# Performance work log

Hardware: AMD Instinct MI355X
Metric: run time of the kernel (lower is better)

Reference implementation:

```python
import jax, jax.numpy as jnp
import numpy as np

B, D, H, L, A, NH = 32768, 512, 512, 64, 4, 4
HD = L // NH  # head dim
TEMPS = jnp.array([1.5, 0.5, 1.0, 0.8], dtype=jnp.float32)  # explorer/exploiter/validator/integrator


def setup_inputs() -> dict:
    key = jax.random.key(0)
    ks = jax.random.split(key, 32)
    s = 0.05
    n = lambda k, shp: jax.random.normal(k, shp, dtype=jnp.float32) * s
    return {
        'x': jax.random.normal(ks[0], (B, D), dtype=jnp.float32),
        'eps': jax.random.normal(ks[1], (B, A, L), dtype=jnp.float32),
        'W1': n(ks[2], (H, D)), 'b1': n(ks[3], (H,)),
        'W2': n(ks[4], (H, H)), 'b2': n(ks[5], (H,)),
        'muW': n(ks[6], (A, L, H)), 'mub': n(ks[7], (A, L)),
        'lvW': n(ks[8], (A, L, H)), 'lvb': n(ks[9], (A, L)),
        'Wqkv': n(ks[10], (3 * L, L)), 'bqkv': n(ks[11], (3 * L,)),
        'Wo': n(ks[12], (L, L)), 'bo': n(ks[13], (L,)),
        'Wc': n(ks[14], (L, A * L)), 'bc': n(ks[15], (L,)),
        'Wd1': n(ks[16], (H, L)), 'bd1': n(ks[17], (H,)),
        'Wd2': n(ks[18], (H, H)), 'bd2': n(ks[19], (H,)),
        'Wd3': n(ks[20], (D, H)), 'bd3': n(ks[21], (D,)),
    }


def reference(x, eps, W1, b1, W2, b2, muW, mub, lvW, lvb,
              Wqkv, bqkv, Wo, bo, Wc, bc, Wd1, bd1, Wd2, bd2, Wd3, bd3):
    b = x.shape[0]
    # shared encoder backbone: Linear-ReLU-Linear-ReLU
    h = jax.nn.relu(x @ W1.T + b1)
    h = jax.nn.relu(h @ W2.T + b2)
    # per-agent heads, batched over agent axis a
    mus = jnp.einsum('bh,alh->bal', h, muW) + mub                      # (B,A,L)
    logvars = jnp.einsum('bh,alh->bal', h, lvW) + lvb + jnp.log(TEMPS)[:, None]
    std = jnp.exp(0.5 * logvars)
    z = mus + eps * std * TEMPS[:, None]                               # (B,A,L)
    # multihead self-attention across the A agents (seq_len = A)
    qkv = z @ Wqkv.T + bqkv                                            # (B,A,3L)
    q, k, v = jnp.split(qkv, 3, axis=-1)
    q = q.reshape(b, A, NH, HD)
    k = k.reshape(b, A, NH, HD)
    v = v.reshape(b, A, NH, HD)
    scores = jnp.einsum('bqnh,bknh->bnqk', q, k) / jnp.sqrt(jnp.float32(HD))
    attn = jax.nn.softmax(scores, axis=-1)
    ctx = jnp.einsum('bnqk,bknh->bqnh', attn, v).reshape(b, A, L)
    z_att = ctx @ Wo.T + bo                                            # (B,A,L)
    # consensus over flattened agent latents
    z_consensus = z_att.reshape(b, A * L) @ Wc.T + bc                  # (B,L)

    def decode(zz):
        d = jax.nn.relu(zz @ Wd1.T + bd1)
        d = jax.nn.relu(d @ Wd2.T + bd2)
        return d @ Wd3.T + bd3

    x_recon = decode(z_consensus)                                      # (B,D)
    agent_recons = decode(z)                                           # (B,A,D)
    # stack consensus recon with per-agent recons: (B, A+1, D)
    return jnp.concatenate([x_recon[:, None, :], agent_recons], axis=1)
```

## Files before the change

### kernel.cpp

```cpp
#include <hip/hip_runtime.h>

typedef __bf16 bf16_t;
typedef __bf16 bf16x8 __attribute__((ext_vector_type(8)));
typedef __bf16 bf16x4 __attribute__((ext_vector_type(4)));
typedef float  f32x4  __attribute__((ext_vector_type(4)));

#define MFMA16(a,b,c) __builtin_amdgcn_mfma_f32_16x16x32_bf16((a),(b),(c),0,0,0)
#define GLOBAL_AS __attribute__((address_space(1)))
#define LDS_AS    __attribute__((address_space(3)))

__device__ __forceinline__ bf16x8 lds_read8(const bf16_t* base, int row, int k, int rowB) {
    int byte = row * rowB + (k << 1);
    byte ^= ((row & 7) << 4);
    return *(const bf16x8*)((const char*)base + byte);
}
__device__ __forceinline__ void lds_write8B(bf16_t* base, int row, int col, int rowB, bf16x4 v) {
    int byte = row * rowB + (col << 1);
    byte ^= ((row & 7) << 4);
    *(bf16x4*)((char*)base + byte) = v;
}
__device__ __forceinline__ bf16x4 lds_read8B(const bf16_t* base, int row, int col, int rowB) {
    int byte = row * rowB + (col << 1);
    byte ^= ((row & 7) << 4);
    return *(const bf16x4*)((const char*)base + byte);
}
__device__ __forceinline__ void lds_write1(bf16_t* base, int row, int col, int rowB, float v) {
    int byte = row * rowB + (col << 1);
    byte ^= ((row & 7) << 4);
    *(bf16_t*)((char*)base + byte) = (bf16_t)v;
}
__device__ __forceinline__ void lds_write16B(bf16_t* base, int row, int colbyte, int rowB, bf16x8 v) {
    int byte = row * rowB + colbyte;
    byte ^= ((row & 7) << 4);
    *(bf16x8*)((char*)base + byte) = v;
}
__device__ __forceinline__ bf16x8 lds_read16B(const bf16_t* base, int row, int colbyte, int rowB) {
    int byte = row * rowB + colbyte;
    byte ^= ((row & 7) << 4);
    return *(const bf16x8*)((const char*)base + byte);
}

__device__ __forceinline__ void gload_lds16(const void* g, void* l) {
    __builtin_amdgcn_global_load_lds((const GLOBAL_AS void*)g, (LDS_AS void*)l, 16, 0, 0);
}
__device__ __forceinline__ void stageW(const bf16_t* __restrict__ Wt, int tile,
                                       char* wbuf, int bufIdx, int wave, int lane) {
    const char* s = (const char*)Wt + (size_t)tile * 32768 + wave * 4096 + lane * 16;
    char* d = wbuf + bufIdx * 32768 + wave * 4096;
#pragma unroll
    for (int c = 0; c < 4; ++c)
        gload_lds16(s + c * 1024, d + c * 1024);
}

template<int NS, bool CONT, int TB>
__device__ __forceinline__ void layer_gl(f32x4 (&acc)[4][4],
    const bf16_t* act, char* wbuf,
    const bf16_t* __restrict__ Wt, const bf16_t* __restrict__ Wn,
    int wave, int lane, int n0, int l15, int lhi)
{
#pragma unroll
    for (int s = 0; s < NS; ++s) {
        if (s == NS - 1 && !CONT) {
            asm volatile("s_waitcnt vmcnt(0)" ::: "memory");
        } else {
            asm volatile("s_waitcnt vmcnt(4)" ::: "memory");
        }
        __builtin_amdgcn_s_barrier();
        if (s + 2 < NS)  stageW(Wt, s + 2,      wbuf, (TB + s + 2) % 3, wave, lane);
        else if (CONT)   stageW(Wn, s + 2 - NS, wbuf, (TB + s + 2) % 3, wave, lane);
        const char* bb = wbuf + ((TB + s) % 3) * 32768 + lhi * 8192;
        bf16x8 a[4], b[4];
#pragma unroll
        for (int cf = 0; cf < 4; ++cf)
            b[cf] = *(const bf16x8*)(bb + (n0 + cf * 16 + l15) * 16);
#pragma unroll
        for (int rf = 0; rf < 4; ++rf)
            a[rf] = lds_read8(act, rf * 16 + l15, s * 32 + lhi * 8, 1024);
#pragma unroll
        for (int rf = 0; rf < 4; ++rf)
#pragma unroll
            for (int cf = 0; cf < 4; ++cf)
                acc[rf][cf] = MFMA16(b[cf], a[rf], acc[rf][cf]);
    }
}

__device__ __forceinline__ void zero4(f32x4 (&acc)[4][4]) {
#pragma unroll
    for (int rf = 0; rf < 4; ++rf)
#pragma unroll
        for (int cf = 0; cf < 4; ++cf)
            acc[rf][cf] = f32x4{0.f, 0.f, 0.f, 0.f};
}

template<bool RELU>
__device__ __forceinline__ void epi_lds(const f32x4 (&acc)[4][4], const float* __restrict__ bias,
    bf16_t* dst, int rowB, int n0, int l15, int lhi)
{
#pragma unroll
    for (int cf = 0; cf < 4; ++cf) {
        const int c0 = n0 + cf * 16 + lhi * 4;
        float4 b4 = *(const float4*)(bias + c0);
#pragma unroll
        for (int rf = 0; rf < 4; ++rf) {
            float v0 = acc[rf][cf][0] + b4.x;
            float v1 = acc[rf][cf][1] + b4.y;
            float v2 = acc[rf][cf][2] + b4.z;
            float v3 = acc[rf][cf][3] + b4.w;
            if (RELU) {
                v0 = fmaxf(v0, 0.f); v1 = fmaxf(v1, 0.f);
                v2 = fmaxf(v2, 0.f); v3 = fmaxf(v3, 0.f);
            }
            bf16x4 p = { (bf16_t)v0, (bf16_t)v1, (bf16_t)v2, (bf16_t)v3 };
            lds_write8B(dst, rf * 16 + l15, c0, rowB, p);
        }
    }
}

__device__ __forceinline__ void epi_global(const f32x4 (&acc)[4][4], const float* __restrict__ bias,
    float* __restrict__ out, long row0, int n0, int l15, int lhi)
{
#pragma unroll
    for (int cf = 0; cf < 4; ++cf) {
        const int c0 = n0 + cf * 16 + lhi * 4;
        float4 b4 = *(const float4*)(bias + c0);
#pragma unroll
        for (int rf = 0; rf < 4; ++rf) {
            float4 o = { acc[rf][cf][0] + b4.x, acc[rf][cf][1] + b4.y,
                         acc[rf][cf][2] + b4.z, acc[rf][cf][3] + b4.w };
            *(float4*)(out + (row0 + rf * 16 + l15) * 512 + c0) = o;
        }
    }
}

__device__ __forceinline__ void decode_tile(int m, int& n, int& k) {
    int s = m >> 14, r = m & 16383;
    int kg = r >> 12, q = r & 4095;
    n = q >> 3;
    k = (s << 5) + (kg << 3) + (q & 7);
}
__global__ __launch_bounds__(256) void cast_kernel(
    const float* __restrict__ W1, const float* __restrict__ W2,
    const float* __restrict__ muW, const float* __restrict__ lvW,
    const float* __restrict__ Wqkv, const float* __restrict__ Wo,
    const float* __restrict__ Wc, const float* __restrict__ Wd1,
    const float* __restrict__ Wd2, const float* __restrict__ Wd3,
    bf16_t* __restrict__ dst)
{
    int i = blockIdx.x * 256 + threadIdx.x;
    float val;
    int n, k;
    if (i < 262144) {
        decode_tile(i, n, k);                     val = W1[n * 512 + k];
    } else if (i < 524288) {
        decode_tile(i - 262144, n, k);            val = W2[n * 512 + k];
    } else if (i < 786432) {
        decode_tile(i - 524288, n, k);
        val = (n < 256) ? muW[n * 512 + k] : lvW[(n - 256) * 512 + k];
    } else if (i < 798720) { val = Wqkv[i - 786432]; }
    else if (i < 802816)   { val = Wo[i - 798720]; }
    else if (i < 819200)   { val = Wc[i - 802816]; }
    else if (i < 851968) {
        decode_tile(i - 819200, n, k);            val = Wd1[n * 64 + k];
    } else if (i < 1114112) {
        decode_tile(i - 851968, n, k);            val = Wd2[n * 512 + k];
    } else {
        decode_tile(i - 1114112, n, k);           val = Wd3[n * 512 + k];
    }
    dst[i] = (bf16_t)val;
}

__global__ __launch_bounds__(512, 2) void enc_kernel(
    const float* __restrict__ x, const float* __restrict__ eps,
    const bf16_t* __restrict__ W1t, const float* __restrict__ b1,
    const bf16_t* __restrict__ W2t, const float* __restrict__ b2,
    const bf16_t* __restrict__ Ht,  const float* __restrict__ mub,
    const float* __restrict__ lvb,  bf16_t* __restrict__ zout)
{
    __shared__ bf16_t act[64 * 512];
    __shared__ alignas(16) char wbuf[3 * 32768];
    const int t = threadIdx.x;
    const int wave = t >> 6, lane = t & 63, l15 = lane & 15, lhi = lane >> 4;
    const int n0 = wave * 64;
    const size_t r0 = (size_t)blockIdx.x * 64;

    stageW(W1t, 0, wbuf, 0, wave, lane);
    stageW(W1t, 1, wbuf, 1, wave, lane);

    for (int it = 0; it < 16; ++it) {
        int flat = it * 512 + t;
        int row = flat >> 7, c4 = flat & 127;
        float4 v = ((const float4*)(x + (r0 + row) * 512))[c4];
        bf16x4 h = { (bf16_t)v.x, (bf16_t)v.y, (bf16_t)v.z, (bf16_t)v.w };
        int byte = (row << 10) + (c4 << 3);
        byte ^= ((row & 7) << 4);
        *(bf16x4*)((char*)act + byte) = h;
    }
    asm volatile("s_waitcnt lgkmcnt(0)" ::: "memory");

    f32x4 acc[4][4];
    zero4(acc);
    layer_gl<16, true, 0>(acc, act, wbuf, W1t, W2t, wave, lane, n0, l15, lhi);
    __builtin_amdgcn_s_barrier();
    epi_lds<true>(acc, b1, act, 1024, n0, l15, lhi);
    asm volatile("s_waitcnt lgkmcnt(0)" ::: "memory");
    __builtin_amdgcn_s_barrier();

    zero4(acc);
    layer_gl<16, true, 1>(acc, act, wbuf, W2t, Ht, wave, lane, n0, l15, lhi);
    __builtin_amdgcn_s_barrier();
    epi_lds<true>(acc, b2, act, 1024, n0, l15, lhi);
    asm volatile("s_waitcnt lgkmcnt(0)" ::: "memory");
    __builtin_amdgcn_s_barrier();

    zero4(acc);
    layer_gl<16, false, 2>(acc, act, wbuf, Ht, (const bf16_t*)nullptr, wave, lane, n0, l15, lhi);
    __builtin_amdgcn_s_barrier();
    epi_lds<false>(acc, (n0 < 256) ? mub : (lvb - 256), act, 1024, n0, l15, lhi);
    asm volatile("s_waitcnt lgkmcnt(0)" ::: "memory");
    __builtin_amdgcn_s_barrier();

    const int cc = (t & 63) * 4;
    const int ag = cc >> 6;
    const float tp = (ag == 0) ? 1.8371173070873836f
                   : (ag == 1) ? 0.35355339059327373f
                   : (ag == 2) ? 1.0f
                               : 0.7155417527999327f;
    const int rb = t >> 6;
    for (int it = 0; it < 8; ++it) {
        int row = it * 8 + rb;
        bf16x4 mu4 = lds_read8B(act, row, cc, 1024);
        bf16x4 lv4 = lds_read8B(act, row, cc + 256, 1024);
        float4 ep4 = *(const float4*)(eps + (r0 + row) * 256 + cc);
        bf16x4 zo;
        zo[0] = (bf16_t)fmaf(ep4.x * tp, expf(0.5f * (float)lv4[0]), (float)mu4[0]);
        zo[1] = (bf16_t)fmaf(ep4.y * tp, expf(0.5f * (float)lv4[1]), (float)mu4[1]);
        zo[2] = (bf16_t)fmaf(ep4.z * tp, expf(0.5f * (float)lv4[2]), (float)mu4[2]);
        zo[3] = (bf16_t)fmaf(ep4.w * tp, expf(0.5f * (float)lv4[3]), (float)mu4[3]);
        *(bf16x4*)(zout + (r0 + row) * 256 + cc) = zo;
    }
}

__global__ __launch_bounds__(512) void attn_kernel(
    const bf16_t* __restrict__ z,
    const bf16_t* __restrict__ Wqkvb, const float* __restrict__ bqkv,
    const bf16_t* __restrict__ Wob,   const float* __restrict__ bo,
    const bf16_t* __restrict__ Wcb,   const float* __restrict__ bc,
    bf16_t* __restrict__ zcb)
{
    __shared__ bf16_t zt[256 * 64];
    __shared__ bf16_t qt[256 * 192];
    const int t = threadIdx.x;
    const size_t s0 = (size_t)blockIdx.x * 64;

    for (int it = 0; it < 4; ++it) {
        int ch = it * 512 + t;
        int r = ch >> 3, cc = ch & 7;
        bf16x8 v = *(const bf16x8*)(z + s0 * 256 + r * 64 + cc * 8);
        lds_write16B(zt, r, cc * 16, 128, v);
    }
    __syncthreads();
    const int wave = t >> 6, lane = t & 63, l15 = lane & 15, lhi = lane >> 4;
    const int rbase = wave * 32;

    for (int cc = 0; cc < 4; ++cc) {
        f32x4 acc[2][3] = {};
#pragma unroll
        for (int ks = 0; ks < 2; ++ks) {
            int k = ks * 32 + lhi * 8;
            bf16x8 a0 = lds_read8(zt, rbase + l15, k, 128);
            bf16x8 a1 = lds_read8(zt, rbase + 16 + l15, k, 128);
#pragma unroll
            for (int cf = 0; cf < 3; ++cf) {
                bf16x8 b = *(const bf16x8*)(Wqkvb + (cc * 48 + cf * 16 + l15) * 64 + k);
                acc[0][cf] = MFMA16(a0, b, acc[0][cf]);
                acc[1][cf] = MFMA16(a1, b, acc[1][cf]);
            }
        }
#pragma unroll
        for (int cf = 0; cf < 3; ++cf) {
            int col = cc * 48 + cf * 16 + l15;
            float bs = bqkv[col];
#pragma unroll
            for (int rf = 0; rf < 2; ++rf)
#pragma unroll
                for (int r = 0; r < 4; ++r)
                    lds_write1(qt, rbase + rf * 16 + lhi * 4 + r, col, 384, acc[rf][cf][r] + bs);
        }
    }
    __syncthreads();

    if (t < 256) {
        const int sl = t >> 2, head = t & 3;
        bf16x8 qv[4][2], kv[4][2], vv[4][2];
#pragma unroll
        for (int a2 = 0; a2 < 4; ++a2) {
            int r = sl * 4 + a2;
#pragma unroll
            for (int i = 0; i < 2; ++i) {
                qv[a2][i] = lds_read16B(qt, r, head * 32 + 16 * i, 384);
                kv[a2][i] = lds_read16B(qt, r, 128 + head * 32 + 16 * i, 384);
                vv[a2][i] = lds_read16B(qt, r, 256 + head * 32 + 16 * i, 384);
            }
        }
        float sc[4][4];
#pragma unroll
        for (int qa = 0; qa < 4; ++qa)
#pragma unroll
            for (int ka = 0; ka < 4; ++ka) {
                float s = 0.f;
#pragma unroll
                for (int i = 0; i < 2; ++i)
#pragma unroll
                    for (int j = 0; j < 8; ++j)
                        s += (float)qv[qa][i][j] * (float)kv[ka][i][j];
                sc[qa][ka] = s * 0.25f;
            }
#pragma unroll
        for (int qa = 0; qa < 4; ++qa) {
            float m = fmaxf(fmaxf(sc[qa][0], sc[qa][1]), fmaxf(sc[qa][2], sc[qa][3]));
            float e[4], sum = 0.f;
#pragma unroll
            for (int ka = 0; ka < 4; ++ka) { e[ka] = expf(sc[qa][ka] - m); sum += e[ka]; }
            float inv = 1.f / sum;
#pragma unroll
            for (int i = 0; i < 2; ++i) {
                bf16x8 cv;
#pragma unroll
                for (int j = 0; j < 8; ++j) {
                    float cval = 0.f;
#pragma unroll
                    for (int ka = 0; ka < 4; ++ka) cval += e[ka] * inv * (float)vv[ka][i][j];
                    cv[j] = (bf16_t)cval;
                }
                lds_write16B(zt, sl * 4 + qa, head * 32 + 16 * i, 128, cv);
            }
        }
    }
    __syncthreads();

    {
        f32x4 acc[2][4] = {};
#pragma unroll
        for (int ks = 0; ks < 2; ++ks) {
            int k = ks * 32 + lhi * 8;
            bf16x8 a0 = lds_read8(zt, rbase + l15, k, 128);
            bf16x8 a1 = lds_read8(zt, rbase + 16 + l15, k, 128);
#pragma unroll
            for (int cf = 0; cf < 4; ++cf) {
                bf16x8 b = *(const bf16x8*)(Wob + (cf * 16 + l15) * 64 + k);
                acc[0][cf] = MFMA16(a0, b, acc[0][cf]);
                acc[1][cf] = MFMA16(a1, b, acc[1][cf]);
            }
        }
        __syncthreads();
#pragma unroll
        for (int cf = 0; cf < 4; ++cf) {
            int col = cf * 16 + l15;
            float bs = bo[col];
#pragma unroll
            for (int rf = 0; rf < 2; ++rf)
#pragma unroll
                for (int r = 0; r < 4; ++r)
                    lds_write1(qt, rbase + rf * 16 + lhi * 4 + r, col, 128, acc[rf][cf][r] + bs);
        }
    }
    __syncthreads();

    {
        f32x4 acc2[2] = {};
        const int rfw = wave >> 1, cbase = (wave & 1) * 2;
        const int srow = rfw * 16 + l15;
#pragma unroll
        for (int ks = 0; ks < 8; ++ks) {
            int k = ks * 32 + lhi * 8;
            int byte = (srow << 9) + (k << 1);
            byte ^= ((((srow << 2) + (k >> 6)) & 7) << 4);
            bf16x8 a = *(const bf16x8*)((const char*)qt + byte);
#pragma unroll
            for (int i = 0; i < 2; ++i) {
                bf16x8 b = *(const bf16x8*)(Wcb + ((cbase + i) * 16 + l15) * 256 + k);
                acc2[i] = MFMA16(a, b, acc2[i]);
            }
        }
#pragma unroll
        for (int i = 0; i < 2; ++i) {
            int col = (cbase + i) * 16 + l15;
            float bs = bc[col];
#pragma unroll
            for (int r = 0; r < 4; ++r) {
                int s = (int)(s0) + rfw * 16 + lhi * 4 + r;
                zcb[(size_t)s * 64 + col] = (bf16_t)(acc2[i][r] + bs);
            }
        }
    }
}

__global__ __launch_bounds__(512, 2) void dec_kernel(
    const bf16_t* __restrict__ z, const bf16_t* __restrict__ zc,
    const bf16_t* __restrict__ Wd1t, const float* __restrict__ bd1,
    const bf16_t* __restrict__ Wd2t, const float* __restrict__ bd2,
    const bf16_t* __restrict__ Wd3t, const float* __restrict__ bd3,
    float* __restrict__ out)
{
    __shared__ bf16_t act[64 * 512];
    __shared__ alignas(16) char wbuf[3 * 32768];
    const int t = threadIdx.x;
    const int wave = t >> 6, lane = t & 63, l15 = lane & 15, lhi = lane >> 4;
    const int n0 = wave * 64;
    const long r0 = (long)blockIdx.x * 64;

    stageW(Wd1t, 0, wbuf, 0, wave, lane);
    stageW(Wd1t, 1, wbuf, 1, wave, lane);

    {
        int row = t >> 3, ch = t & 7;
        long rg = r0 + row;
        int s5 = (int)(rg / 5), j = (int)(rg - (long)s5 * 5);
        const bf16_t* src = (j == 0) ? (zc + (size_t)s5 * 64)
                                     : (z + (size_t)s5 * 256 + (j - 1) * 64);
        bf16x8 v = *(const bf16x8*)(src + ch * 8);
        int byte = (row << 10) + (ch << 4);
        byte ^= ((row & 7) << 4);
        *(bf16x8*)((char*)act + byte) = v;
    }
    asm volatile("s_waitcnt lgkmcnt(0)" ::: "memory");

    f32x4 acc[4][4];
    zero4(acc);
    layer_gl<2, true, 0>(acc, act, wbuf, Wd1t, Wd2t, wave, lane, n0, l15, lhi);
    __builtin_amdgcn_s_barrier();
    epi_lds<true>(acc, bd1, act, 1024, n0, l15, lhi);
    asm volatile("s_waitcnt lgkmcnt(0)" ::: "memory");
    __builtin_amdgcn_s_barrier();

    zero4(acc);
    layer_gl<16, true, 2>(acc, act, wbuf, Wd2t, Wd3t, wave, lane, n0, l15, lhi);
    __builtin_amdgcn_s_barrier();
    epi_lds<true>(acc, bd2, act, 1024, n0, l15, lhi);
    asm volatile("s_waitcnt lgkmcnt(0)" ::: "memory");
    __builtin_amdgcn_s_barrier();

    zero4(acc);
    layer_gl<16, false, 0>(acc, act, wbuf, Wd3t, (const bf16_t*)nullptr, wave, lane, n0, l15, lhi);
    epi_global(acc, bd3, out, r0, n0, l15, lhi);
}

extern "C" void kernel_launch(void* const* d_in, const int* in_sizes, int n_in,
                              void* d_out, int out_size, void* d_ws, size_t ws_size,
                              hipStream_t stream) {
    const float* x    = (const float*)d_in[0];
    const float* eps  = (const float*)d_in[1];
    const float* W1   = (const float*)d_in[2];
    const float* b1   = (const float*)d_in[3];
    const float* W2   = (const float*)d_in[4];
    const float* b2   = (const float*)d_in[5];
    const float* muW  = (const float*)d_in[6];
    const float* mub  = (const float*)d_in[7];
    const float* lvW  = (const float*)d_in[8];
    const float* lvb  = (const float*)d_in[9];
    const float* Wqkv = (const float*)d_in[10];
    const float* bqkv = (const float*)d_in[11];
    const float* Wo   = (const float*)d_in[12];
    const float* bo   = (const float*)d_in[13];
    const float* Wc   = (const float*)d_in[14];
    const float* bc   = (const float*)d_in[15];
    const float* Wd1  = (const float*)d_in[16];
    const float* bd1  = (const float*)d_in[17];
    const float* Wd2  = (const float*)d_in[18];
    const float* bd2  = (const float*)d_in[19];
    const float* Wd3  = (const float*)d_in[20];
    const float* bd3  = (const float*)d_in[21];
    float* out = (float*)d_out;

    bf16_t* wsb  = (bf16_t*)d_ws;
    bf16_t* W1t  = wsb + 0;
    bf16_t* W2t  = wsb + 262144;
    bf16_t* Ht   = wsb + 524288;
    bf16_t* Wqkvb= wsb + 786432;
    bf16_t* Wob  = wsb + 798720;
    bf16_t* Wcb  = wsb + 802816;
    bf16_t* Wd1t = wsb + 819200;
    bf16_t* Wd2t = wsb + 851968;
    bf16_t* Wd3t = wsb + 1114112;
    bf16_t* zbuf = wsb + 1376256;
    bf16_t* zcb  = wsb + 9764864;

    cast_kernel<<<dim3(5376), dim3(256), 0, stream>>>(
        W1, W2, muW, lvW, Wqkv, Wo, Wc, Wd1, Wd2, Wd3, wsb);
    enc_kernel<<<dim3(512), dim3(512), 0, stream>>>(
        x, eps, W1t, b1, W2t, b2, Ht, mub, lvb, zbuf);
    attn_kernel<<<dim3(512), dim3(512), 0, stream>>>(
        zbuf, Wqkvb, bqkv, Wob, bo, Wcb, bc, zcb);
    dec_kernel<<<dim3(2560), dim3(512), 0, stream>>>(
        zbuf, zcb, Wd1t, bd1, Wd2t, bd2, Wd3t, bd3, out);
}
```

Baseline: 435.4 us.

## Repack weight tiles row-contiguous, preload biases into accumulators, raise MFMA priority

Changes the bf16 weight tile packing so each output row's 32 k-values are stored contiguously (64B per row) instead of in four k-group planes, and updates the LDS read addressing to match. Biases are loaded once into registers at kernel start and used to initialise the accumulators, which removes the bias adds and bias loads from the epilogues. The MFMA block is wrapped in s_setprio so waves doing math are scheduled ahead of waves issuing loads. The new LDS layout may change bank-conflict behaviour, and the preloaded biases add register pressure.

New measurement: 496.6 us. 14.0% more time.

```diff
diff --git a/kernel.cpp b/kernel.cpp
--- a/kernel.cpp
+++ b/kernel.cpp
@@ -50,6 +50,15 @@
 #pragma unroll
     for (int c = 0; c < 4; ++c)
         gload_lds16(s + c * 1024, d + c * 1024);
+}
+
+__device__ __forceinline__ void init_acc(f32x4 (&acc)[4][4], const float4 (&b4)[4]) {
+#pragma unroll
+    for (int cf = 0; cf < 4; ++cf) {
+        f32x4 v = { b4[cf].x, b4[cf].y, b4[cf].z, b4[cf].w };
+#pragma unroll
+        for (int rf = 0; rf < 4; ++rf) acc[rf][cf] = v;
+    }
 }
 
 template<int NS, bool CONT, int TB>
@@ -68,44 +77,35 @@
         __builtin_amdgcn_s_barrier();
         if (s + 2 < NS)  stageW(Wt, s + 2,      wbuf, (TB + s + 2) % 3, wave, lane);
         else if (CONT)   stageW(Wn, s + 2 - NS, wbuf, (TB + s + 2) % 3, wave, lane);
-        const char* bb = wbuf + ((TB + s) % 3) * 32768 + lhi * 8192;
+        const char* bb = wbuf + ((TB + s) % 3) * 32768;
         bf16x8 a[4], b[4];
 #pragma unroll
         for (int cf = 0; cf < 4; ++cf)
-            b[cf] = *(const bf16x8*)(bb + (n0 + cf * 16 + l15) * 16);
+            b[cf] = *(const bf16x8*)(bb + (n0 + cf * 16 + l15) * 64 + lhi * 16);
 #pragma unroll
         for (int rf = 0; rf < 4; ++rf)
             a[rf] = lds_read8(act, rf * 16 + l15, s * 32 + lhi * 8, 1024);
+        __builtin_amdgcn_s_setprio(1);
 #pragma unroll
         for (int rf = 0; rf < 4; ++rf)
 #pragma unroll
             for (int cf = 0; cf < 4; ++cf)
                 acc[rf][cf] = MFMA16(b[cf], a[rf], acc[rf][cf]);
-    }
-}
-
-__device__ __forceinline__ void zero4(f32x4 (&acc)[4][4]) {
-#pragma unroll
-    for (int rf = 0; rf < 4; ++rf)
-#pragma unroll
-        for (int cf = 0; cf < 4; ++cf)
-            acc[rf][cf] = f32x4{0.f, 0.f, 0.f, 0.f};
+        __builtin_amdgcn_s_setprio(0);
+    }
 }
 
 template<bool RELU>
-__device__ __forceinline__ void epi_lds(const f32x4 (&acc)[4][4], const float* __restrict__ bias,
+__device__ __forceinline__ void epi_lds(const f32x4 (&acc)[4][4],
     bf16_t* dst, int rowB, int n0, int l15, int lhi)
 {
 #pragma unroll
     for (int cf = 0; cf < 4; ++cf) {
         const int c0 = n0 + cf * 16 + lhi * 4;
-        float4 b4 = *(const float4*)(bias + c0);
 #pragma unroll
         for (int rf = 0; rf < 4; ++rf) {
-            float v0 = acc[rf][cf][0] + b4.x;
-            float v1 = acc[rf][cf][1] + b4.y;
-            float v2 = acc[rf][cf][2] + b4.z;
-            float v3 = acc[rf][cf][3] + b4.w;
+            float v0 = acc[rf][cf][0], v1 = acc[rf][cf][1];
+            float v2 = acc[rf][cf][2], v3 = acc[rf][cf][3];
             if (RELU) {
                 v0 = fmaxf(v0, 0.f); v1 = fmaxf(v1, 0.f);
                 v2 = fmaxf(v2, 0.f); v3 = fmaxf(v3, 0.f);
@@ -115,18 +115,16 @@
         }
     }
 }
-
-__device__ __forceinline__ void epi_global(const f32x4 (&acc)[4][4], const float* __restrict__ bias,
+__device__ __forceinline__ void epi_global(const f32x4 (&acc)[4][4],
     float* __restrict__ out, long row0, int n0, int l15, int lhi)
 {
 #pragma unroll
     for (int cf = 0; cf < 4; ++cf) {
         const int c0 = n0 + cf * 16 + lhi * 4;
-        float4 b4 = *(const float4*)(bias + c0);
 #pragma unroll
         for (int rf = 0; rf < 4; ++rf) {
-            float4 o = { acc[rf][cf][0] + b4.x, acc[rf][cf][1] + b4.y,
-                         acc[rf][cf][2] + b4.z, acc[rf][cf][3] + b4.w };
+            float4 o = { acc[rf][cf][0], acc[rf][cf][1],
+                         acc[rf][cf][2], acc[rf][cf][3] };
             *(float4*)(out + (row0 + rf * 16 + l15) * 512 + c0) = o;
         }
     }
@@ -134,9 +132,8 @@
 
 __device__ __forceinline__ void decode_tile(int m, int& n, int& k) {
     int s = m >> 14, r = m & 16383;
-    int kg = r >> 12, q = r & 4095;
-    n = q >> 3;
-    k = (s << 5) + (kg << 3) + (q & 7);
+    n = r >> 5;
+    k = (s << 5) + (((r >> 3) & 3) << 3) + (r & 7);
 }
 __global__ __launch_bounds__(256) void cast_kernel(
     const float* __restrict__ W1, const float* __restrict__ W2,
@@ -183,6 +180,18 @@
     const int n0 = wave * 64;
     const size_t r0 = (size_t)blockIdx.x * 64;
 
+    float4 b14[4], b24[4], bh4[4];
+    {
+        const float* hb = (n0 < 256) ? mub : (lvb - 256);
+        const int cb = n0 + lhi * 4;
+#pragma unroll
+        for (int cf = 0; cf < 4; ++cf) {
+            b14[cf] = *(const float4*)(b1 + cb + cf * 16);
+            b24[cf] = *(const float4*)(b2 + cb + cf * 16);
+            bh4[cf] = *(const float4*)(hb + cb + cf * 16);
+        }
+    }
+
     stageW(W1t, 0, wbuf, 0, wave, lane);
     stageW(W1t, 1, wbuf, 1, wave, lane);
 
@@ -198,24 +207,24 @@
     asm volatile("s_waitcnt lgkmcnt(0)" ::: "memory");
 
     f32x4 acc[4][4];
-    zero4(acc);
+    init_acc(acc, b14);
     layer_gl<16, true, 0>(acc, act, wbuf, W1t, W2t, wave, lane, n0, l15, lhi);
     __builtin_amdgcn_s_barrier();
-    epi_lds<true>(acc, b1, act, 1024, n0, l15, lhi);
-    asm volatile("s_waitcnt lgkmcnt(0)" ::: "memory");
-    __builtin_amdgcn_s_barrier();
-
-    zero4(acc);
+    epi_lds<true>(acc, act, 1024, n0, l15, lhi);
+    asm volatile("s_waitcnt lgkmcnt(0)" ::: "memory");
+    __builtin_amdgcn_s_barrier();
+
+    init_acc(acc, b24);
     layer_gl<16, true, 1>(acc, act, wbuf, W2t, Ht, wave, lane, n0, l15, lhi);
     __builtin_amdgcn_s_barrier();
-    epi_lds<true>(acc, b2, act, 1024, n0, l15, lhi);
-    asm volatile("s_waitcnt lgkmcnt(0)" ::: "memory");
-    __builtin_amdgcn_s_barrier();
-
-    zero4(acc);
+    epi_lds<true>(acc, act, 1024, n0, l15, lhi);
+    asm volatile("s_waitcnt lgkmcnt(0)" ::: "memory");
+    __builtin_amdgcn_s_barrier();
+
+    init_acc(acc, bh4);
     layer_gl<16, false, 2>(acc, act, wbuf, Ht, (const bf16_t*)nullptr, wave, lane, n0, l15, lhi);
     __builtin_amdgcn_s_barrier();
-    epi_lds<false>(acc, (n0 < 256) ? mub : (lvb - 256), act, 1024, n0, l15, lhi);
+    epi_lds<false>(acc, act, 1024, n0, l15, lhi);
     asm volatile("s_waitcnt lgkmcnt(0)" ::: "memory");
     __builtin_amdgcn_s_barrier();
 
@@ -409,6 +418,17 @@
     const int n0 = wave * 64;
     const long r0 = (long)blockIdx.x * 64;
 
+    float4 bd14[4], bd24[4], bd34[4];
+    {
+        const int cb = n0 + lhi * 4;
+#pragma unroll
+        for (int cf = 0; cf < 4; ++cf) {
+            bd14[cf] = *(const float4*)(bd1 + cb + cf * 16);
+            bd24[cf] = *(const float4*)(bd2 + cb + cf * 16);
+            bd34[cf] = *(const float4*)(bd3 + cb + cf * 16);
+        }
+    }
+
     stageW(Wd1t, 0, wbuf, 0, wave, lane);
     stageW(Wd1t, 1, wbuf, 1, wave, lane);
 
@@ -426,23 +446,23 @@
     asm volatile("s_waitcnt lgkmcnt(0)" ::: "memory");
 
     f32x4 acc[4][4];
-    zero4(acc);
+    init_acc(acc, bd14);
     layer_gl<2, true, 0>(acc, act, wbuf, Wd1t, Wd2t, wave, lane, n0, l15, lhi);
     __builtin_amdgcn_s_barrier();
-    epi_lds<true>(acc, bd1, act, 1024, n0, l15, lhi);
-    asm volatile("s_waitcnt lgkmcnt(0)" ::: "memory");
-    __builtin_amdgcn_s_barrier();
-
-    zero4(acc);
+    epi_lds<true>(acc, act, 1024, n0, l15, lhi);
+    asm volatile("s_waitcnt lgkmcnt(0)" ::: "memory");
+    __builtin_amdgcn_s_barrier();
+
+    init_acc(acc, bd24);
     layer_gl<16, true, 2>(acc, act, wbuf, Wd2t, Wd3t, wave, lane, n0, l15, lhi);
     __builtin_amdgcn_s_barrier();
-    epi_lds<true>(acc, bd2, act, 1024, n0, l15, lhi);
-    asm volatile("s_waitcnt lgkmcnt(0)" ::: "memory");
-    __builtin_amdgcn_s_barrier();
-
-    zero4(acc);
+    epi_lds<true>(acc, act, 1024, n0, l15, lhi);
+    asm volatile("s_waitcnt lgkmcnt(0)" ::: "memory");
+    __builtin_amdgcn_s_barrier();
+
+    init_acc(acc, bd34);
     layer_gl<16, false, 0>(acc, act, wbuf, Wd3t, (const bf16_t*)nullptr, wave, lane, n0, l15, lhi);
-    epi_global(acc, bd3, out, r0, n0, l15, lhi);
+    epi_global(acc, out, r0, n0, l15, lhi);
 }
 
 extern "C" void kernel_launch(void* const* d_in, const int* in_sizes, int n_in,
```
